# Optimization experiments

Hardware: AMD Instinct MI355X
Metric: run time of the kernel (lower is better)

## Reference

```python
import jax, jax.numpy as jnp
import numpy as np

GAMMA = 0.95  # usage decay from NTM.__init__

def setup_inputs() -> dict:
    key = jax.random.key(0)
    ks = jax.random.split(key, 16)
    B, N, M, R, U, Din = 256, 32768, 64, 4, 256, 512
    Dc = Din + R * M  # controller input = x concat prev read vectors
    s = 0.02
    x = jax.random.normal(ks[0], (B, Din), jnp.float32)
    A = jax.random.normal(ks[1], (N, M), jnp.float32) * 0.1
    wr_prev = jax.nn.softmax(jax.random.normal(ks[2], (R, B, N), jnp.float32), axis=-1)
    wu_prev = jax.random.uniform(ks[3], (B, N), jnp.float32)
    read_prev = jax.random.normal(ks[4], (R, B, M), jnp.float32) * 0.1
    h = jax.random.normal(ks[5], (B, U), jnp.float32) * 0.1
    c = jax.random.normal(ks[6], (B, U), jnp.float32) * 0.1
    W = jax.random.normal(ks[7], (Dc, 4 * U), jnp.float32) * s
    Uw = jax.random.normal(ks[8], (U, 4 * U), jnp.float32) * s
    b = jnp.zeros((4 * U,), jnp.float32)
    Wk = jax.random.normal(ks[9], (R, U, M), jnp.float32) * s
    bk = jnp.zeros((R, M), jnp.float32)
    Wa = jax.random.normal(ks[10], (U, R), jnp.float32) * s
    ba = jnp.zeros((R,), jnp.float32)
    return dict(x=x, A=A, wr_prev=wr_prev, wu_prev=wu_prev, read_prev=read_prev,
                h=h, c=c, W=W, Uw=Uw, b=b, Wk=Wk, bk=bk, Wa=Wa, ba=ba)

def reference(x, A, wr_prev, wu_prev, read_prev, h, c, W, Uw, b, Wk, bk, Wa, ba):
    B, N = wu_prev.shape
    R, _, M = read_prev.shape
    # ---- controller (single LSTM cell step, keras gate order i,f,g,o) ----
    ctrl_in = jnp.concatenate([x, read_prev.transpose(1, 0, 2).reshape(B, -1)], axis=-1)
    gates = ctrl_in @ W + h @ Uw + b
    gi, gf, gg, go = jnp.split(gates, 4, axis=-1)
    c_new = jax.nn.sigmoid(gf) * c + jax.nn.sigmoid(gi) * jnp.tanh(gg)
    h_new = jax.nn.sigmoid(go) * jnp.tanh(c_new)  # controller_output [B,U]
    # ---- least-used weights from previous usage ----
    least = jnp.argmin(wu_prev, axis=-1)                       # [B]
    wlu = jax.nn.one_hot(least, N, dtype=wu_prev.dtype)        # [B,N]
    # ---- read heads: cosine-similarity content addressing ----
    kt = jnp.tanh(jnp.einsum('bu,rum->rbm', h_new, Wk) + bk[:, None, :])  # [R,B,M]
    inner = jnp.einsum('rbm,nm->rbn', kt, A)                   # [R,B,N]
    knorm = jnp.linalg.norm(kt, axis=-1)                       # [R,B]
    anorm = jnp.linalg.norm(A, axis=-1)                        # [N]
    Ksim = inner / (knorm[..., None] * anorm[None, None, :] + 1e-16)
    wr = jax.nn.softmax(Ksim, axis=-1)                         # [R,B,N]
    # ---- write head: gated mix of prev read weights and least-used ----
    alpha = jax.nn.sigmoid(jnp.tanh(h_new @ Wa + ba))          # [B,R]
    a = alpha.T[:, :, None]                                    # [R,B,1]
    ww = a * wr_prev + (1.0 - a) * wlu[None]                   # [R,B,N]
    # ---- usage update ----
    wu = GAMMA * wu_prev + jnp.sum(wr + ww, axis=0)            # [B,N]
    # ---- memory: erase least-used row(s), then tanh additive writes ----
    erase = 1.0 - jnp.max(wlu, axis=0)                         # [N]
    A_new = A * erase[:, None]
    for r in range(R):  # small fixed head count
        A_new = jnp.tanh(A_new + jnp.einsum('bn,bm->nm', ww[r], kt[r]))
    # ---- reads and output ----
    reads = jnp.einsum('rbn,nm->rbm', wr, A_new)               # [R,B,M]
    out = jnp.concatenate([h_new, reads.transpose(1, 0, 2).reshape(B, -1)], axis=-1)
    return out
```

## Files before the change

kernel.cpp:

```cpp
#include <hip/hip_runtime.h>
#include <hip/hip_bf16.h>
#include <stdint.h>

#define B_   256
#define N_   32768
#define M_   64
#define R_   4
#define U_   256
#define DIN_ 512
#define DC_  768
#define J4_  1024
#define Q_   1024
#define NPART_ 32

typedef __attribute__((ext_vector_type(8))) short short8v;
typedef __attribute__((ext_vector_type(4))) float f32x4;

__device__ __forceinline__ float sigm(float x){ return 1.f/(1.f+__expf(-x)); }
__device__ __forceinline__ float tanh_f(float x){ float e=__expf(2.f*x); return 1.f - 2.f/(e+1.f); }
__device__ __forceinline__ unsigned short f2bf(float x){
    unsigned u = __float_as_uint(x);
    u += 0x7FFFu + ((u>>16)&1u);
    return (unsigned short)(u>>16);
}

__global__ __launch_bounds__(256) void k_zero(int* lflag, float* l){
    int i = blockIdx.x*256 + threadIdx.x;
    if(i < N_) lflag[i] = 0;
    if(i < Q_) l[i] = 0.f;
}

__global__ __launch_bounds__(256) void k_anorm(const float* A, float* anorm, unsigned short* A_bf){
    int n = blockIdx.x*4 + (threadIdx.x>>6);
    int lane = threadIdx.x & 63;
    float v = A[n*64 + lane];
    A_bf[n*64 + lane] = f2bf(v);
    float s = v*v;
    #pragma unroll
    for(int m=1;m<64;m<<=1) s += __shfl_xor(s, m, 64);
    if(lane==0) anorm[n] = sqrtf(s);
}

__global__ __launch_bounds__(256) void k_argmin(const float* wu, int* least, int* lflag){
    __shared__ float sv[256]; __shared__ int si[256];
    int b = blockIdx.x, t = threadIdx.x;
    const float* row = wu + (size_t)b*N_;
    float bv = 3.4e38f; int bi = 0;
    for(int n=t; n<N_; n+=256){ float v = row[n]; if(v < bv){ bv=v; bi=n; } }
    sv[t]=bv; si[t]=bi; __syncthreads();
    for(int s=128;s>0;s>>=1){
        if(t<s){
            float ov=sv[t+s]; int oi=si[t+s];
            if(ov<sv[t] || (ov==sv[t] && oi<si[t])){ sv[t]=ov; si[t]=oi; }
        }
        __syncthreads();
    }
    if(t==0){ least[b]=si[0]; lflag[si[0]]=1; }
}

__global__ __launch_bounds__(256) void k_lstm_gemm(const float* x, const float* rp, const float* h,
                                                   const float* W, const float* Uw, float* gpart){
    __shared__ float s_in[8*128];
    int bt = blockIdx.x >> 3, ks = blockIdx.x & 7;
    int b0 = bt*8, t = threadIdx.x;
    for(int i=t; i<1024; i+=256){
        int bb = i>>7, kk = i&127, k = ks*128 + kk, b = b0+bb;
        float v;
        if(k < DIN_) v = x[b*DIN_ + k];
        else if(k < DC_){ int k2 = k - DIN_; v = rp[(k2>>6)*(B_*M_) + b*M_ + (k2&63)]; }
        else v = h[b*U_ + (k-DC_)];
        s_in[bb*128 + kk] = v;
    }
    __syncthreads();
    float4 acc[8];
    #pragma unroll
    for(int i=0;i<8;i++) acc[i] = make_float4(0.f,0.f,0.f,0.f);
    const float* Wsel; int krel;
    if(ks < 6){ Wsel = W; krel = ks*128; } else { Wsel = Uw; krel = ks*128 - DC_; }
    int j0 = t*4;
    for(int kk=0; kk<128; kk++){
        float4 w = *(const float4*)(Wsel + (size_t)(krel+kk)*J4_ + j0);
        #pragma unroll
        for(int bb=0;bb<8;bb++){
            float s = s_in[bb*128 + kk];
            acc[bb].x += s*w.x; acc[bb].y += s*w.y; acc[bb].z += s*w.z; acc[bb].w += s*w.w;
        }
    }
    #pragma unroll
    for(int bb=0;bb<8;bb++)
        *(float4*)(gpart + (size_t)ks*(B_*J4_) + (size_t)(b0+bb)*J4_ + j0) = acc[bb];
}

__global__ __launch_bounds__(256) void k_lstm_act(const float* gpart, const float* bias, const float* c,
                                                  float* h_new, float* out){
    int b = blockIdx.x, u = threadIdx.x;
    float gi=bias[u], gf=bias[256+u], gg=bias[512+u], go=bias[768+u];
    #pragma unroll
    for(int s=0;s<8;s++){
        const float* gp = gpart + (size_t)s*(B_*J4_) + (size_t)b*J4_;
        gi += gp[u]; gf += gp[256+u]; gg += gp[512+u]; go += gp[768+u];
    }
    float cn = sigm(gf)*c[b*U_+u] + sigm(gi)*tanh_f(gg);
    float hn = sigm(go)*tanh_f(cn);
    h_new[b*U_+u] = hn;
    out[(size_t)b*512 + u] = hn;
}

__global__ __launch_bounds__(64) void k_kta(const float* h_new, const float* Wk, const float* bk,
                                            const float* Wa, const float* ba,
                                            float* kt, unsigned short* kt_bf, float* aktw,
                                            float* alpha, float* knorm){
    __shared__ float h_l[256];
    int r = blockIdx.x >> 8, b = blockIdx.x & 255, m = threadIdx.x;
    for(int i=m;i<256;i+=64) h_l[i] = h_new[b*U_ + i];
    __syncthreads();
    float acc = bk[r*64 + m];
    const float* wkp = Wk + (size_t)r*U_*M_ + m;
    for(int u=0;u<256;u++) acc += h_l[u] * wkp[u*64];
    float k = tanh_f(acc);
    float s = k*k;
    #pragma unroll
    for(int mm=1;mm<64;mm<<=1) s += __shfl_xor(s, mm, 64);
    float pa = 0.f;
    #pragma unroll
    for(int uu=0; uu<4; uu++){ int u = m*4+uu; pa += h_l[u]*Wa[u*R_ + r]; }
    #pragma unroll
    for(int mm=1;mm<64;mm<<=1) pa += __shfl_xor(pa, mm, 64);
    float al = sigm(tanh_f(pa + ba[r]));
    int q = r*256 + b;
    kt[q*64 + m]    = k;
    kt_bf[q*64 + m] = f2bf(k);
    aktw[q*64 + m]  = al*k;
    if(m==0){ knorm[q] = sqrtf(s); alpha[q] = al; }
}

__global__ __launch_bounds__(256,2) void k_Ggemm(const float* wrp, const float* aktw, float* G){
    __shared__ float wr_l[32*256];
    __shared__ float akt_l[32*64];
    int r = blockIdx.x >> 7, nt = blockIdx.x & 127;
    int nb = nt*256, t = threadIdx.x;
    int tm = t & 15, tn = t >> 4;
    const float* wbase = wrp  + (size_t)r*((size_t)B_*N_);
    const float* abase = aktw + (size_t)r*(B_*M_);
    float4 acc[16];
    #pragma unroll
    for(int i=0;i<16;i++) acc[i]=make_float4(0.f,0.f,0.f,0.f);
    for(int tile=0; tile<8; tile++){
        int bb0 = tile*32;
        __syncthreads();
        for(int i=t; i<2048; i+=256){
            int kk = i>>6, cc = i&63;
            *(float4*)(wr_l + kk*256 + cc*4) = *(const float4*)(wbase + (size_t)(bb0+kk)*N_ + nb + cc*4);
        }
        for(int i=t; i<512; i+=256){
            int kk = i>>4, cc = i&15;
            *(float4*)(akt_l + kk*64 + cc*4) = *(const float4*)(abase + (bb0+kk)*64 + cc*4);
        }
        __syncthreads();
        #pragma unroll 4
        for(int kk=0; kk<32; kk++){
            float4 af = *(const float4*)(akt_l + kk*64 + tm*4);
            float4 w0 = *(const float4*)(wr_l + kk*256 + tn*16);
            float4 w1 = *(const float4*)(wr_l + kk*256 + tn*16 + 4);
            float4 w2 = *(const float4*)(wr_l + kk*256 + tn*16 + 8);
            float4 w3 = *(const float4*)(wr_l + kk*256 + tn*16 + 12);
#define GFMA(I, WV) { acc[I].x += (WV)*af.x; acc[I].y += (WV)*af.y; acc[I].z += (WV)*af.z; acc[I].w += (WV)*af.w; }
            GFMA(0,w0.x) GFMA(1,w0.y) GFMA(2,w0.z) GFMA(3,w0.w)
            GFMA(4,w1.x) GFMA(5,w1.y) GFMA(6,w1.z) GFMA(7,w1.w)
            GFMA(8,w2.x) GFMA(9,w2.y) GFMA(10,w2.z) GFMA(11,w2.w)
            GFMA(12,w3.x) GFMA(13,w3.y) GFMA(14,w3.z) GFMA(15,w3.w)
#undef GFMA
        }
    }
    float* gout = G + (size_t)r*((size_t)N_*64);
    #pragma unroll
    for(int i=0;i<16;i++)
        *(float4*)(gout + (size_t)(nb + tn*16 + i)*64 + tm*4) = acc[i];
}

__global__ __launch_bounds__(64) void k_scatter(const float* kt, const float* alpha, const int* least, float* G){
    int r = blockIdx.x >> 8, b = blockIdx.x & 255, m = threadIdx.x;
    int q = r*256+b;
    float v = (1.f - alpha[q]) * kt[q*64 + m];
    int row = least[b];
    atomicAdd(G + (size_t)r*((size_t)N_*64) + (size_t)row*64 + m, v);
}

__global__ __launch_bounds__(256) void k_Aupd(const float* A, const float* G, const int* lflag, float* Anew){
    int i4 = blockIdx.x*256 + threadIdx.x;
    int n = i4 >> 4;
    float er = lflag[n] ? 0.f : 1.f;
    float4 a = ((const float4*)A)[i4];
    float4 v = make_float4(a.x*er, a.y*er, a.z*er, a.w*er);
    #pragma unroll
    for(int r=0;r<4;r++){
        float4 g = ((const float4*)G)[(size_t)r*524288 + i4];
        v.x = tanh_f(v.x+g.x); v.y = tanh_f(v.y+g.y); v.z = tanh_f(v.z+g.z); v.w = tanh_f(v.w+g.w);
    }
    ((float4*)Anew)[i4] = v;
}

__global__ __launch_bounds__(256) void k_vt(const float* Anew, unsigned short* Vt){
    __shared__ __align__(16) unsigned short lt[4096];
    int n0 = blockIdx.x*64, t = threadIdx.x;
    int row = t>>2, cb = t&3;
    #pragma unroll
    for(int i=0;i<4;i++){
        int cidx = cb*4 + i;
        float4 f = *(const float4*)(Anew + (size_t)(n0+row)*64 + cidx*4);
        int m0 = cidx*4;
        lt[(m0  )*64 + row] = f2bf(f.x);
        lt[(m0+1)*64 + row] = f2bf(f.y);
        lt[(m0+2)*64 + row] = f2bf(f.z);
        lt[(m0+3)*64 + row] = f2bf(f.w);
    }
    __syncthreads();
    int mr = t>>2;
    #pragma unroll
    for(int cc=0; cc<2; cc++){
        int c = (t&3) + cc*4;
        uint4 v = *(const uint4*)(lt + mr*64 + c*8);
        *(uint4*)(Vt + (size_t)mr*N_ + n0 + c*8) = v;
    }
}

__global__ __launch_bounds__(256) void k_attn(const unsigned short* kt_bf, const unsigned short* A_bf,
                                              const unsigned short* Vt, const float* knorm,
                                              const float* anorm, float* part, float* l){
    __shared__ __align__(16) unsigned short Pl[64*256];
    int nc = blockIdx.x >> 4, qt = blockIdx.x & 15;
    int qb = qt*64, nb = nc*1024;
    int lane = threadIdx.x & 63, w = threadIdx.x >> 6;
    int r16 = lane & 15, hq = lane >> 4;
    const short8v* kp = (const short8v*)(kt_bf + (size_t)(qb + w*16 + r16)*64 + hq*8);
    short8v ka0 = kp[0], ka1 = kp[4];
    float kn[4];
    #pragma unroll
    for(int j=0;j<4;j++) kn[j] = knorm[qb + w*16 + hq*4 + j];
    f32x4 O[4];
    #pragma unroll
    for(int mt=0;mt<4;mt++) O[mt] = (f32x4){0.f,0.f,0.f,0.f};
    float lp[4] = {0.f,0.f,0.f,0.f};
    int g2 = (r16 >> 2) & 3;

    for(int c=0; c<4; c++){
        int n0c = nb + c*256;
        __syncthreads();
        for(int nt=0; nt<16; nt++){
            int ntb = n0c + nt*16;
            const short8v* bp = (const short8v*)(A_bf + (size_t)(ntb + r16)*64 + hq*8);
            f32x4 acc = (f32x4){0.f,0.f,0.f,0.f};
            acc = __builtin_amdgcn_mfma_f32_16x16x32_bf16(ka0, bp[0], acc, 0, 0, 0);
            acc = __builtin_amdgcn_mfma_f32_16x16x32_bf16(ka1, bp[4], acc, 0, 0, 0);
            float an = anorm[ntb + r16];
            unsigned um[4];
            #pragma unroll
            for(int j=0;j<4;j++){
                float p = __expf(__fdividef(acc[j], kn[j]*an + 1e-16f));
                lp[j] += p;
                um[j] = (unsigned)f2bf(p);
            }
            int nl = nt*16 + (r16 & ~1);
            #pragma unroll
            for(int j=0;j<4;j++){
                unsigned up = __shfl_xor((int)um[j], 1, 64);
                if((lane & 1) == 0){
                    unsigned word = um[j] | (up << 16);
                    int byteoff = (w*16 + hq*4 + j)*512 + ((nl ^ (hq<<4)) << 1);
                    *(unsigned*)((char*)Pl + byteoff) = word;
                }
            }
        }
        __syncthreads();
        #pragma unroll 2
        for(int ks=0; ks<8; ks++){
            short8v pa = *(const short8v*)((const char*)Pl +
                          ((w*16 + r16)*512 + (((ks*32 + hq*8) ^ (g2<<4)) << 1)));
            #pragma unroll
            for(int mt=0; mt<4; mt++){
                const short8v* vp = (const short8v*)(Vt + (size_t)(mt*16 + r16)*N_ + n0c + ks*32 + hq*8);
                O[mt] = __builtin_amdgcn_mfma_f32_16x16x32_bf16(pa, vp[0], O[mt], 0, 0, 0);
            }
        }
    }
    #pragma unroll
    for(int mt=0; mt<4; mt++)
        #pragma unroll
        for(int j=0;j<4;j++)
            part[((size_t)nc*Q_ + (qb + w*16 + hq*4 + j))*64 + mt*16 + r16] = O[mt][j];
    #pragma unroll
    for(int j=0;j<4;j++){
        #pragma unroll
        for(int m2=1;m2<16;m2<<=1) lp[j] += __shfl_xor(lp[j], m2, 64);
        if(r16 == 0) atomicAdd(l + qb + w*16 + hq*4 + j, lp[j]);
    }
}

__global__ __launch_bounds__(256) void k_reduce(const float* part, const float* l, float* out){
    int tg = blockIdx.x*256 + threadIdx.x;
    int q = tg >> 6, m = tg & 63;
    float s = 0.f;
    for(int cc=0;cc<NPART_;cc++) s += part[(size_t)cc*(Q_*64) + tg];
    float val = s / l[q];
    int r = q >> 8, b = q & 255;
    out[(size_t)b*512 + 256 + r*64 + m] = val;
}

extern "C" void kernel_launch(void* const* d_in, const int* in_sizes, int n_in,
                              void* d_out, int out_size, void* d_ws, size_t ws_size,
                              hipStream_t stream) {
    const float* x        = (const float*)d_in[0];
    const float* A        = (const float*)d_in[1];
    const float* wr_prev  = (const float*)d_in[2];
    const float* wu_prev  = (const float*)d_in[3];
    const float* read_prev= (const float*)d_in[4];
    const float* h        = (const float*)d_in[5];
    const float* c        = (const float*)d_in[6];
    const float* W        = (const float*)d_in[7];
    const float* Uw       = (const float*)d_in[8];
    const float* bvec     = (const float*)d_in[9];
    const float* Wk       = (const float*)d_in[10];
    const float* bk       = (const float*)d_in[11];
    const float* Wa       = (const float*)d_in[12];
    const float* ba       = (const float*)d_in[13];
    float* out = (float*)d_out;

    char* wsp = (char*)d_ws;
    float* G      = (float*)(wsp);
    float* Anew   = (float*)(wsp + 33554432);
    float* part   = (float*)(wsp + 41943040);
    unsigned short* A_bf  = (unsigned short*)(wsp + 50331648);
    unsigned short* Vt_bf = (unsigned short*)(wsp + 54525952);
    unsigned short* kt_bf = (unsigned short*)(wsp + 58720256);
    float* h_new  = (float*)(wsp + 58851328);
    float* kt     = (float*)(wsp + 59113472);
    float* aktw   = (float*)(wsp + 59375616);
    float* alpha  = (float*)(wsp + 59637760);
    float* knorm  = (float*)(wsp + 59641856);
    float* anorm  = (float*)(wsp + 59645952);
    int*   lflag  = (int*)  (wsp + 59777024);
    float* l      = (float*)(wsp + 59908096);
    int*   least  = (int*)  (wsp + 59912192);

    k_zero     <<<128, 256, 0, stream>>>(lflag, l);
    k_anorm    <<<8192,256, 0, stream>>>(A, anorm, A_bf);
    k_argmin   <<<256, 256, 0, stream>>>(wu_prev, least, lflag);
    k_lstm_gemm<<<256, 256, 0, stream>>>(x, read_prev, h, W, Uw, G);
    k_lstm_act <<<256, 256, 0, stream>>>(G, bvec, c, h_new, out);
    k_kta      <<<1024, 64, 0, stream>>>(h_new, Wk, bk, Wa, ba, kt, kt_bf, aktw, alpha, knorm);
    k_Ggemm    <<<512, 256, 0, stream>>>(wr_prev, aktw, G);
    k_scatter  <<<1024, 64, 0, stream>>>(kt, alpha, least, G);
    k_Aupd     <<<2048,256, 0, stream>>>(A, G, lflag, Anew);
    k_vt       <<<512, 256, 0, stream>>>(Anew, Vt_bf);
    k_attn     <<<512, 256, 0, stream>>>(kt_bf, A_bf, Vt_bf, knorm, anorm, part, l);
    k_reduce   <<<256, 256, 0, stream>>>(part, l, out);
}
```

Baseline: 494.9 us.

## Fuse write-outer-product GEMM, scatter, memory update and transpose into one bf16 MFMA kernel

Replaces the fp32 FMA G-gemm, the atomic scatter, the A update and the Vt transpose kernels with a single kernel. It computes the per-head outer products with bf16 MFMA, adds the least-used scatter terms inline, applies the tanh chain, and writes the transposed bf16 Vt straight from shared memory. This removes the 32 MB G intermediate round trip and several launches. It also doubles the attention partition count, so k_attn runs twice as many blocks, and splits the LSTM GEMM K dimension into 16 slices for more parallelism. The write GEMM inputs (wr_prev and alpha*k) are now rounded to bf16, which adds precision loss.

```diff
diff --git a/kernel.cpp b/kernel.cpp
--- a/kernel.cpp
+++ b/kernel.cpp
@@ -11,7 +11,7 @@
 #define DC_  768
 #define J4_  1024
 #define Q_   1024
-#define NPART_ 32
+#define NPART_ 64
 
 typedef __attribute__((ext_vector_type(8))) short short8v;
 typedef __attribute__((ext_vector_type(4))) float f32x4;
@@ -60,29 +60,31 @@
 
 __global__ __launch_bounds__(256) void k_lstm_gemm(const float* x, const float* rp, const float* h,
                                                    const float* W, const float* Uw, float* gpart){
-    __shared__ float s_in[8*128];
-    int bt = blockIdx.x >> 3, ks = blockIdx.x & 7;
+    __shared__ float s_in[8*64];
+    int bt = blockIdx.x >> 4, ks = blockIdx.x & 15;
     int b0 = bt*8, t = threadIdx.x;
-    for(int i=t; i<1024; i+=256){
-        int bb = i>>7, kk = i&127, k = ks*128 + kk, b = b0+bb;
+    #pragma unroll
+    for(int i=t; i<512; i+=256){
+        int bb = i>>6, kk = i&63, b = b0+bb;
         float v;
-        if(k < DIN_) v = x[b*DIN_ + k];
-        else if(k < DC_){ int k2 = k - DIN_; v = rp[(k2>>6)*(B_*M_) + b*M_ + (k2&63)]; }
-        else v = h[b*U_ + (k-DC_)];
-        s_in[bb*128 + kk] = v;
+        if(ks < 8)       v = x[b*DIN_ + ks*64 + kk];
+        else if(ks < 12) v = rp[(size_t)(ks-8)*(B_*M_) + b*64 + kk];
+        else             v = h[b*U_ + (ks-12)*64 + kk];
+        s_in[bb*64 + kk] = v;
     }
     __syncthreads();
     float4 acc[8];
     #pragma unroll
     for(int i=0;i<8;i++) acc[i] = make_float4(0.f,0.f,0.f,0.f);
     const float* Wsel; int krel;
-    if(ks < 6){ Wsel = W; krel = ks*128; } else { Wsel = Uw; krel = ks*128 - DC_; }
+    if(ks < 12){ Wsel = W; krel = ks*64; } else { Wsel = Uw; krel = (ks-12)*64; }
     int j0 = t*4;
-    for(int kk=0; kk<128; kk++){
+    #pragma unroll 4
+    for(int kk=0; kk<64; kk++){
         float4 w = *(const float4*)(Wsel + (size_t)(krel+kk)*J4_ + j0);
         #pragma unroll
         for(int bb=0;bb<8;bb++){
-            float s = s_in[bb*128 + kk];
+            float s = s_in[bb*64 + kk];
             acc[bb].x += s*w.x; acc[bb].y += s*w.y; acc[bb].z += s*w.z; acc[bb].w += s*w.w;
         }
     }
@@ -96,7 +98,7 @@
     int b = blockIdx.x, u = threadIdx.x;
     float gi=bias[u], gf=bias[256+u], gg=bias[512+u], go=bias[768+u];
     #pragma unroll
-    for(int s=0;s<8;s++){
+    for(int s=0;s<16;s++){
         const float* gp = gpart + (size_t)s*(B_*J4_) + (size_t)b*J4_;
         gi += gp[u]; gf += gp[256+u]; gg += gp[512+u]; go += gp[768+u];
     }
@@ -108,7 +110,7 @@
 
 __global__ __launch_bounds__(64) void k_kta(const float* h_new, const float* Wk, const float* bk,
                                             const float* Wa, const float* ba,
-                                            float* kt, unsigned short* kt_bf, float* aktw,
+                                            float* kt, unsigned short* kt_bf, unsigned short* aktT,
                                             float* alpha, float* knorm){
     __shared__ float h_l[256];
     int r = blockIdx.x >> 8, b = blockIdx.x & 255, m = threadIdx.x;
@@ -130,97 +132,102 @@
     int q = r*256 + b;
     kt[q*64 + m]    = k;
     kt_bf[q*64 + m] = f2bf(k);
-    aktw[q*64 + m]  = al*k;
+    aktT[(size_t)(r*64 + m)*256 + b] = f2bf(al*k);
     if(m==0){ knorm[q] = sqrtf(s); alpha[q] = al; }
 }
 
-__global__ __launch_bounds__(256,2) void k_Ggemm(const float* wrp, const float* aktw, float* G){
-    __shared__ float wr_l[32*256];
-    __shared__ float akt_l[32*64];
-    int r = blockIdx.x >> 7, nt = blockIdx.x & 127;
-    int nb = nt*256, t = threadIdx.x;
-    int tm = t & 15, tn = t >> 4;
-    const float* wbase = wrp  + (size_t)r*((size_t)B_*N_);
-    const float* abase = aktw + (size_t)r*(B_*M_);
-    float4 acc[16];
-    #pragma unroll
-    for(int i=0;i<16;i++) acc[i]=make_float4(0.f,0.f,0.f,0.f);
-    for(int tile=0; tile<8; tile++){
-        int bb0 = tile*32;
-        __syncthreads();
-        for(int i=t; i<2048; i+=256){
-            int kk = i>>6, cc = i&63;
-            *(float4*)(wr_l + kk*256 + cc*4) = *(const float4*)(wbase + (size_t)(bb0+kk)*N_ + nb + cc*4);
-        }
-        for(int i=t; i<512; i+=256){
-            int kk = i>>4, cc = i&15;
-            *(float4*)(akt_l + kk*64 + cc*4) = *(const float4*)(abase + (bb0+kk)*64 + cc*4);
-        }
-        __syncthreads();
-        #pragma unroll 4
-        for(int kk=0; kk<32; kk++){
-            float4 af = *(const float4*)(akt_l + kk*64 + tm*4);
-            float4 w0 = *(const float4*)(wr_l + kk*256 + tn*16);
-            float4 w1 = *(const float4*)(wr_l + kk*256 + tn*16 + 4);
-            float4 w2 = *(const float4*)(wr_l + kk*256 + tn*16 + 8);
-            float4 w3 = *(const float4*)(wr_l + kk*256 + tn*16 + 12);
-#define GFMA(I, WV) { acc[I].x += (WV)*af.x; acc[I].y += (WV)*af.y; acc[I].z += (WV)*af.z; acc[I].w += (WV)*af.w; }
-            GFMA(0,w0.x) GFMA(1,w0.y) GFMA(2,w0.z) GFMA(3,w0.w)
-            GFMA(4,w1.x) GFMA(5,w1.y) GFMA(6,w1.z) GFMA(7,w1.w)
-            GFMA(8,w2.x) GFMA(9,w2.y) GFMA(10,w2.z) GFMA(11,w2.w)
-            GFMA(12,w3.x) GFMA(13,w3.y) GFMA(14,w3.z) GFMA(15,w3.w)
-#undef GFMA
-        }
-    }
-    float* gout = G + (size_t)r*((size_t)N_*64);
-    #pragma unroll
-    for(int i=0;i<16;i++)
-        *(float4*)(gout + (size_t)(nb + tn*16 + i)*64 + tm*4) = acc[i];
-}
-
-__global__ __launch_bounds__(64) void k_scatter(const float* kt, const float* alpha, const int* least, float* G){
-    int r = blockIdx.x >> 8, b = blockIdx.x & 255, m = threadIdx.x;
-    int q = r*256+b;
-    float v = (1.f - alpha[q]) * kt[q*64 + m];
-    int row = least[b];
-    atomicAdd(G + (size_t)r*((size_t)N_*64) + (size_t)row*64 + m, v);
-}
-
-__global__ __launch_bounds__(256) void k_Aupd(const float* A, const float* G, const int* lflag, float* Anew){
-    int i4 = blockIdx.x*256 + threadIdx.x;
-    int n = i4 >> 4;
-    float er = lflag[n] ? 0.f : 1.f;
-    float4 a = ((const float4*)A)[i4];
-    float4 v = make_float4(a.x*er, a.y*er, a.z*er, a.w*er);
-    #pragma unroll
-    for(int r=0;r<4;r++){
-        float4 g = ((const float4*)G)[(size_t)r*524288 + i4];
-        v.x = tanh_f(v.x+g.x); v.y = tanh_f(v.y+g.y); v.z = tanh_f(v.z+g.z); v.w = tanh_f(v.w+g.w);
-    }
-    ((float4*)Anew)[i4] = v;
-}
-
-__global__ __launch_bounds__(256) void k_vt(const float* Anew, unsigned short* Vt){
-    __shared__ __align__(16) unsigned short lt[4096];
-    int n0 = blockIdx.x*64, t = threadIdx.x;
-    int row = t>>2, cb = t&3;
-    #pragma unroll
-    for(int i=0;i<4;i++){
-        int cidx = cb*4 + i;
-        float4 f = *(const float4*)(Anew + (size_t)(n0+row)*64 + cidx*4);
-        int m0 = cidx*4;
-        lt[(m0  )*64 + row] = f2bf(f.x);
-        lt[(m0+1)*64 + row] = f2bf(f.y);
-        lt[(m0+2)*64 + row] = f2bf(f.z);
-        lt[(m0+3)*64 + row] = f2bf(f.w);
+__global__ __launch_bounds__(256) void k_Gfused(const float* wrp, const unsigned short* aktT,
+                                                const float* A, const float* kt, const float* alpha,
+                                                const int* least, const int* lflag,
+                                                unsigned short* Vt){
+    __shared__ __align__(16) char wrl[16384];
+    __shared__ __align__(16) char aktl[16384];
+    __shared__ int least_l[256];
+    int nb = blockIdx.x*64, t = threadIdx.x;
+    int w = t>>6, lane = t&63;
+    int r16 = lane&15, hq = lane>>4;
+    for(int i=t;i<256;i+=256) least_l[i] = least[i];
+
+    f32x4 acc[4][4];
+    #pragma unroll
+    for(int r=0;r<4;r++)
+        #pragma unroll
+        for(int ms=0;ms<4;ms++) acc[r][ms] = (f32x4){0.f,0.f,0.f,0.f};
+
+    int sb = lane>>1, nh = (lane&1)*32;
+    for(int kt8=0; kt8<8; kt8++){
+        int b0 = kt8*32;
+        __syncthreads();
+        const float4* src = (const float4*)(wrp + ((size_t)w*B_ + b0 + sb)*N_ + nb + nh);
+        float4 f[8];
+        #pragma unroll
+        for(int i=0;i<8;i++) f[i] = src[i];
+        const uint4* ap = (const uint4*)(aktT + ((size_t)(w*64 + lane))*256 + b0);
+        uint4 av[4];
+        #pragma unroll
+        for(int c=0;c<4;c++) av[c] = ap[c];
+        #pragma unroll
+        for(int i=0;i<8;i++){
+            float vv[4] = {f[i].x, f[i].y, f[i].z, f[i].w};
+            #pragma unroll
+            for(int c=0;c<4;c++){
+                int n = nh + i*4 + c;
+                *(unsigned short*)(wrl + n*256 + ((w*64 + sb*2) ^ ((n&7)<<4))) = f2bf(vv[c]);
+            }
+        }
+        #pragma unroll
+        for(int c=0;c<4;c++)
+            *(uint4*)(aktl + lane*256 + ((w*64 + c*16) ^ ((lane&7)<<4))) = av[c];
+        __syncthreads();
+        #pragma unroll
+        for(int r=0;r<4;r++){
+            int n = w*16 + r16;
+            short8v af = *(const short8v*)(wrl + n*256 + ((r*64 + hq*16) ^ ((n&7)<<4)));
+            #pragma unroll
+            for(int ms=0;ms<4;ms++){
+                int m = ms*16 + r16;
+                short8v bf = *(const short8v*)(aktl + m*256 + ((r*64 + hq*16) ^ ((m&7)<<4)));
+                acc[r][ms] = __builtin_amdgcn_mfma_f32_16x16x32_bf16(af, bf, acc[r][ms], 0, 0, 0);
+            }
+        }
     }
     __syncthreads();
-    int mr = t>>2;
-    #pragma unroll
-    for(int cc=0; cc<2; cc++){
-        int c = (t&3) + cc*4;
-        uint4 v = *(const uint4*)(lt + mr*64 + c*8);
-        *(uint4*)(Vt + (size_t)mr*N_ + n0 + c*8) = v;
+    #pragma unroll
+    for(int j=0;j<4;j++){
+        int nl = w*16 + hq*4 + j, gn = nb + nl;
+        int fl = lflag[gn];
+        float er = fl ? 0.f : 1.f;
+        float sadd[4][4];
+        #pragma unroll
+        for(int r=0;r<4;r++){ sadd[r][0]=0.f; sadd[r][1]=0.f; sadd[r][2]=0.f; sadd[r][3]=0.f; }
+        if(fl){
+            for(int b=0;b<256;b++){
+                if(least_l[b]==gn){
+                    #pragma unroll
+                    for(int r=0;r<4;r++){
+                        float am = 1.f - alpha[r*256+b];
+                        const float* kp = kt + ((size_t)(r*256+b))*64 + r16;
+                        #pragma unroll
+                        for(int ms=0;ms<4;ms++) sadd[r][ms] += am * kp[ms*16];
+                    }
+                }
+            }
+        }
+        #pragma unroll
+        for(int ms=0;ms<4;ms++){
+            int m = ms*16 + r16;
+            float v = A[(size_t)gn*64 + m] * er;
+            #pragma unroll
+            for(int r=0;r<4;r++) v = tanh_f(v + acc[r][ms][j] + sadd[r][ms]);
+            *(unsigned short*)(wrl + m*128 + ((nl*2) ^ ((m&7)<<4))) = f2bf(v);
+        }
+    }
+    __syncthreads();
+    int m = t>>2, cq = t&3;
+    #pragma unroll
+    for(int hh=0;hh<2;hh++){
+        uint4 v = *(const uint4*)(wrl + m*128 + ((cq*32 + hh*16) ^ ((m&7)<<4)));
+        *(uint4*)(Vt + (size_t)m*N_ + nb + cq*16 + hh*8) = v;
     }
 }
 
@@ -229,7 +236,7 @@
                                               const float* anorm, float* part, float* l){
     __shared__ __align__(16) unsigned short Pl[64*256];
     int nc = blockIdx.x >> 4, qt = blockIdx.x & 15;
-    int qb = qt*64, nb = nc*1024;
+    int qb = qt*64, nb = nc*512;
     int lane = threadIdx.x & 63, w = threadIdx.x >> 6;
     int r16 = lane & 15, hq = lane >> 4;
     const short8v* kp = (const short8v*)(kt_bf + (size_t)(qb + w*16 + r16)*64 + hq*8);
@@ -243,7 +250,7 @@
     float lp[4] = {0.f,0.f,0.f,0.f};
     int g2 = (r16 >> 2) & 3;
 
-    for(int c=0; c<4; c++){
+    for(int c=0; c<2; c++){
         int n0c = nb + c*256;
         __syncthreads();
         for(int nt=0; nt<16; nt++){
@@ -326,32 +333,28 @@
     float* out = (float*)d_out;
 
     char* wsp = (char*)d_ws;
-    float* G      = (float*)(wsp);
-    float* Anew   = (float*)(wsp + 33554432);
-    float* part   = (float*)(wsp + 41943040);
-    unsigned short* A_bf  = (unsigned short*)(wsp + 50331648);
-    unsigned short* Vt_bf = (unsigned short*)(wsp + 54525952);
-    unsigned short* kt_bf = (unsigned short*)(wsp + 58720256);
-    float* h_new  = (float*)(wsp + 58851328);
-    float* kt     = (float*)(wsp + 59113472);
-    float* aktw   = (float*)(wsp + 59375616);
-    float* alpha  = (float*)(wsp + 59637760);
-    float* knorm  = (float*)(wsp + 59641856);
-    float* anorm  = (float*)(wsp + 59645952);
-    int*   lflag  = (int*)  (wsp + 59777024);
-    float* l      = (float*)(wsp + 59908096);
-    int*   least  = (int*)  (wsp + 59912192);
+    float* gpart  = (float*)(wsp);
+    float* part   = (float*)(wsp + 16777216);
+    unsigned short* A_bf  = (unsigned short*)(wsp + 33554432);
+    unsigned short* Vt_bf = (unsigned short*)(wsp + 37748736);
+    unsigned short* aktT  = (unsigned short*)(wsp + 41943040);
+    float* kt     = (float*)(wsp + 42074112);
+    unsigned short* kt_bf = (unsigned short*)(wsp + 42336256);
+    float* h_new  = (float*)(wsp + 42467328);
+    float* alpha  = (float*)(wsp + 42729472);
+    float* knorm  = (float*)(wsp + 42733568);
+    float* anorm  = (float*)(wsp + 42737664);
+    int*   lflag  = (int*)  (wsp + 42868736);
+    float* l      = (float*)(wsp + 42999808);
+    int*   least  = (int*)  (wsp + 43003904);
 
     k_zero     <<<128, 256, 0, stream>>>(lflag, l);
     k_anorm    <<<8192,256, 0, stream>>>(A, anorm, A_bf);
     k_argmin   <<<256, 256, 0, stream>>>(wu_prev, least, lflag);
-    k_lstm_gemm<<<256, 256, 0, stream>>>(x, read_prev, h, W, Uw, G);
-    k_lstm_act <<<256, 256, 0, stream>>>(G, bvec, c, h_new, out);
-    k_kta      <<<1024, 64, 0, stream>>>(h_new, Wk, bk, Wa, ba, kt, kt_bf, aktw, alpha, knorm);
-    k_Ggemm    <<<512, 256, 0, stream>>>(wr_prev, aktw, G);
-    k_scatter  <<<1024, 64, 0, stream>>>(kt, alpha, least, G);
-    k_Aupd     <<<2048,256, 0, stream>>>(A, G, lflag, Anew);
-    k_vt       <<<512, 256, 0, stream>>>(Anew, Vt_bf);
-    k_attn     <<<512, 256, 0, stream>>>(kt_bf, A_bf, Vt_bf, knorm, anorm, part, l);
+    k_lstm_gemm<<<512, 256, 0, stream>>>(x, read_prev, h, W, Uw, gpart);
+    k_lstm_act <<<256, 256, 0, stream>>>(gpart, bvec, c, h_new, out);
+    k_kta      <<<1024, 64, 0, stream>>>(h_new, Wk, bk, Wa, ba, kt, kt_bf, aktT, alpha, knorm);
+    k_Gfused   <<<512, 256, 0, stream>>>(wr_prev, aktT, A, kt, alpha, least, lflag, Vt_bf);
+    k_attn     <<<1024,256, 0, stream>>>(kt_bf, A_bf, Vt_bf, knorm, anorm, part, l);
     k_reduce   <<<256, 256, 0, stream>>>(part, l, out);
 }
```

New measurement: 453.3 us. 1.09x faster.
